# Optimization experiments

Hardware: AMD Instinct MI355X
Metric: run time of the kernel (lower is better)

The kernel has to match this reference:

```python
import jax, jax.numpy as jnp
import numpy as np

N_NODES = 2000
N_EDGES = 40000
DILATION = 2
DC = 32  # dilation_channels
C_IN = 32  # in_channels (= gcn out_channels)


def setup_inputs() -> dict:
    key = jax.random.key(0)
    ks = jax.random.split(key, 8)
    x = jax.random.normal(ks[0], (4, 34, N_NODES, C_IN), jnp.float32)
    edge_index = jax.random.randint(ks[1], (2, N_EDGES), 0, N_NODES, dtype=jnp.int64)
    edge_weight = jax.random.uniform(ks[2], (N_EDGES,), jnp.float32)
    gate1_w = jax.random.normal(ks[3], (DC, C_IN, 1, 2), jnp.float32) * 0.1
    gate1_b = jnp.zeros((DC,), jnp.float32)
    gate2_w = jax.random.normal(ks[4], (DC, C_IN, 1, 2), jnp.float32) * 0.1
    gate2_b = jnp.zeros((DC,), jnp.float32)
    gcn_w = jax.random.normal(ks[5], (DC, C_IN), jnp.float32) * 0.1
    gcn_b = jnp.zeros((C_IN,), jnp.float32)
    return {"x": x, "edge_index": edge_index, "edge_weight": edge_weight,
            "gate1_w": gate1_w, "gate1_b": gate1_b,
            "gate2_w": gate2_w, "gate2_b": gate2_b,
            "gcn_w": gcn_w, "gcn_b": gcn_b}


def _gate_conv(x_nchw, w, b):
    # Conv2d(kernel=(1,2), dilation=DILATION), VALID padding -> acts on time (W) axis
    y = jax.lax.conv_general_dilated(
        x_nchw, w, window_strides=(1, 1), padding='VALID',
        rhs_dilation=(1, DILATION),
        dimension_numbers=('NCHW', 'OIHW', 'NCHW'))
    return y + b[None, :, None, None]


def reference(x, edge_index, edge_weight, gate1_w, gate1_b, gate2_w, gate2_b, gcn_w, gcn_b):
    B, T, N, C = x.shape
    xt = jnp.transpose(x, (0, 3, 2, 1))  # (B, C, N, T)
    g1 = jnp.tanh(_gate_conv(xt, gate1_w, gate1_b))      # (B, DC, N, T')
    g2 = jax.nn.sigmoid(_gate_conv(xt, gate2_w, gate2_b))
    g = g1 * g2
    Tp = g.shape[-1]
    h = jnp.transpose(g, (0, 3, 2, 1)).reshape(B * Tp, N, DC)  # (Bt, N, DC)

    # GCN normalization with self loops (PyG gcn_norm, add_self_loops=True)
    row, col = edge_index[0], edge_index[1]
    loop = jnp.arange(N, dtype=edge_index.dtype)
    row_f = jnp.concatenate([row, loop])
    col_f = jnp.concatenate([col, loop])
    w_f = jnp.concatenate([edge_weight, jnp.ones((N,), edge_weight.dtype)])
    deg = jax.ops.segment_sum(w_f, col_f, num_segments=N)
    dis = jnp.where(deg > 0, jax.lax.rsqrt(deg), 0.0)
    norm = dis[row_f] * w_f * dis[col_f]  # (E+N,)

    hw = jnp.einsum('bnd,de->bne', h, gcn_w)          # (Bt, N, C_IN)
    msgs = hw[:, row_f, :] * norm[None, :, None]      # (Bt, E+N, C_IN)
    out = jnp.zeros_like(hw).at[:, col_f, :].add(msgs) + gcn_b  # scatter over targets

    return out.reshape(B, Tp, N, C_IN)  # (B, T', N, in_channels)
```

## Files before the change

### kernel.cpp

```cpp
#include <hip/hip_runtime.h>
#include <hip/hip_bf16.h>

typedef short short8 __attribute__((ext_vector_type(8)));
typedef float floatx4 __attribute__((ext_vector_type(4)));
typedef unsigned short ushort8_t __attribute__((ext_vector_type(8)));

#define NN 2000
#define NE 40000
#define NB 4
#define T_IN 34
#define TP 32
#define NBT (NB * TP)
#define NPOS (NB * TP * NN)
#define CAP 96


__device__ inline unsigned short f2bf(float x) {
    unsigned int u = __float_as_uint(x);
    u = u + 0x7fff + ((u >> 16) & 1);
    return (unsigned short)(u >> 16);
}
__device__ inline void splitPair(float x0, float x1, unsigned& hi, unsigned& lo) {
    unsigned u0 = __float_as_uint(x0), u1 = __float_as_uint(x1);
    hi = __builtin_amdgcn_perm(u1, u0, 0x07060302u);
    float r0 = x0 - __uint_as_float(u0 & 0xffff0000u);
    float r1 = x1 - __uint_as_float(u1 & 0xffff0000u);
    lo = __builtin_amdgcn_perm(__float_as_uint(r1), __float_as_uint(r0), 0x07060302u);
}
__device__ inline void splitA8(const float* v, short8& hi, short8& lo) {
    union { unsigned u[4]; short8 s; } H, L;
#pragma unroll
    for (int j = 0; j < 4; ++j) {
        unsigned h_, l_;
        splitPair(v[2 * j], v[2 * j + 1], h_, l_);
        H.u[j] = h_; L.u[j] = l_;
    }
    hi = H.s; lo = L.s;
}

__global__ __launch_bounds__(256) void conv_deg_kernel(
        const float* __restrict__ x,
        const float* __restrict__ w1, const float* __restrict__ b1,
        const float* __restrict__ w2, const float* __restrict__ b2,
        unsigned short* __restrict__ h2,
        const int* __restrict__ row, const int* __restrict__ col,
        const float* __restrict__ ew,
        float* __restrict__ deg, int* __restrict__ cursor,
        int2* __restrict__ pcsr) {
    if (blockIdx.x >= 1000) {
        int e = (blockIdx.x - 1000) * 256 + threadIdx.x;
        if (e < NE) {
            int c = col[e], r = row[e];
            float w = ew[e];
            atomicAdd(&deg[c], w);
            int slot = atomicAdd(&cursor[c], 1);
            if (slot < CAP) pcsr[c * CAP + slot] = make_int2(r, __float_as_int(w));
        }
        return;
    }

    int l = threadIdx.x & 63;
    int w = threadIdx.x >> 6;
    int colL = l & 15, q = l >> 4;

    short8 Whi[2][2][2], Wlo[2][2][2];
#pragma unroll
    for (int g = 0; g < 2; ++g) {
        const float* wp = g ? w2 : w1;
#pragma unroll
        for (int d = 0; d < 2; ++d)
#pragma unroll
        for (int tap = 0; tap < 2; ++tap) {
            float wv[8];
#pragma unroll
            for (int j = 0; j < 8; ++j)
                wv[j] = wp[(d * 16 + colL) * 64 + (q * 8 + j) * 2 + tap];
            splitA8(wv, Whi[g][d][tap], Wlo[g][d][tap]);
        }
    }
    float bias[2][2] = { { b1[colL], b1[colL + 16] }, { b2[colL], b2[colL + 16] } };

    for (int i = 0; i < 4; ++i) {
        int tile = blockIdx.x * 16 + w * 4 + i;
        int pos0 = tile * 16;
        int bt = pos0 / 2000;
        int n0 = pos0 - bt * 2000;
        int b_ = bt >> 5, t_ = bt & 31;
        const float* xa = x + (((b_ * T_IN + t_) * NN) + n0 + colL) * 32 + q * 8;
        const float* xb = xa + 2 * NN * 32;
        float va[8], vb[8];
        *(float4*)va       = *(const float4*)xa;
        *(float4*)(va + 4) = *(const float4*)(xa + 4);
        *(float4*)vb       = *(const float4*)xb;
        *(float4*)(vb + 4) = *(const float4*)(xb + 4);
        short8 Ahi0, Alo0, Ahi1, Alo1;
        splitA8(va, Ahi0, Alo0);
        splitA8(vb, Ahi1, Alo1);

        floatx4 acc[2][2];
#pragma unroll
        for (int g = 0; g < 2; ++g)
#pragma unroll
        for (int d = 0; d < 2; ++d) {
            float bv = bias[g][d];
            floatx4 a = { bv, bv, bv, bv };
            a = __builtin_amdgcn_mfma_f32_16x16x32_bf16(Ahi0, Whi[g][d][0], a, 0, 0, 0);
            a = __builtin_amdgcn_mfma_f32_16x16x32_bf16(Ahi1, Whi[g][d][1], a, 0, 0, 0);
            a = __builtin_amdgcn_mfma_f32_16x16x32_bf16(Alo0, Whi[g][d][0], a, 0, 0, 0);
            a = __builtin_amdgcn_mfma_f32_16x16x32_bf16(Alo1, Whi[g][d][1], a, 0, 0, 0);
            a = __builtin_amdgcn_mfma_f32_16x16x32_bf16(Ahi0, Wlo[g][d][0], a, 0, 0, 0);
            a = __builtin_amdgcn_mfma_f32_16x16x32_bf16(Ahi1, Wlo[g][d][1], a, 0, 0, 0);
            acc[g][d] = a;
        }

#pragma unroll
        for (int d = 0; d < 2; ++d)
#pragma unroll
        for (int r = 0; r < 4; ++r) {
            float g1 = acc[0][d][r];
            float g2 = acc[1][d][r];
            float e2 = __expf(2.0f * g1);
            float th = (e2 - 1.0f) / (e2 + 1.0f);
            float sg = 1.0f / (1.0f + __expf(-g2));
            float h = th * sg;
            int n = n0 + q * 4 + r;
            h2[(n * NBT + bt) * 32 + d * 16 + colL] = f2bf(h);
        }
    }
}

__device__ inline void acc8(float2* a2, const ushort8_t& v, float nr) {
    union { ushort8_t s; unsigned u[4]; } U; U.s = v;
#pragma unroll
    for (int j = 0; j < 4; ++j) {
        float2 vv;
        vv.x = __uint_as_float(U.u[j] << 16);
        vv.y = __uint_as_float(U.u[j] & 0xffff0000u);
        a2[j].x += vv.x * nr;
        a2[j].y += vv.y * nr;
    }
}

__global__ __launch_bounds__(256) void agg_gcn_kernel(
        const unsigned short* __restrict__ h2,
        const float* __restrict__ deg, const int* __restrict__ cursor,
        const int2* __restrict__ pcsr,
        const float* __restrict__ gw, const float* __restrict__ gb,
        float* __restrict__ out) {
    __shared__ float st[64 * 36];
    int l = threadIdx.x & 63;
    int wv = threadIdx.x >> 6;
    int b = blockIdx.x;
    int cp = b & 7;
    int n = (b >> 3) * 4 + wv;
    int colL = l & 15, q = l >> 4;

    short8 Bhi[2], Blo[2];
#pragma unroll
    for (int d = 0; d < 2; ++d) {
        float wv8[8];
#pragma unroll
        for (int j = 0; j < 8; ++j)
            wv8[j] = gw[(q * 8 + j) * 32 + d * 16 + colL];
        splitA8(wv8, Bhi[d], Blo[d]);
    }
    float gb0 = gb[colL], gb1 = gb[colL + 16];

    const unsigned short* base = h2 + cp * 512 + l * 8;
    float dn = rsqrtf(deg[n] + 1.0f);
    float w0 = dn * dn;
    float2 a2[4] = { {0,0}, {0,0}, {0,0}, {0,0} };
    {
        ushort8_t sv = *(const ushort8_t*)(base + (size_t)n * 4096);
        acc8(a2, sv, w0);
    }
    int cnt = cursor[n]; if (cnt > CAP) cnt = CAP;
    const int2* slots = pcsr + n * CAP;
    int i = 0;
    for (; i + 8 <= cnt; i += 8) {
        int2 e0 = slots[i],     e1 = slots[i + 1], e2 = slots[i + 2], e3 = slots[i + 3];
        int2 e4 = slots[i + 4], e5 = slots[i + 5], e6 = slots[i + 6], e7 = slots[i + 7];
        float n0 = rsqrtf(deg[e0.x] + 1.0f) * __int_as_float(e0.y) * dn;
        float n1 = rsqrtf(deg[e1.x] + 1.0f) * __int_as_float(e1.y) * dn;
        float n2 = rsqrtf(deg[e2.x] + 1.0f) * __int_as_float(e2.y) * dn;
        float n3 = rsqrtf(deg[e3.x] + 1.0f) * __int_as_float(e3.y) * dn;
        float n4 = rsqrtf(deg[e4.x] + 1.0f) * __int_as_float(e4.y) * dn;
        float n5 = rsqrtf(deg[e5.x] + 1.0f) * __int_as_float(e5.y) * dn;
        float n6 = rsqrtf(deg[e6.x] + 1.0f) * __int_as_float(e6.y) * dn;
        float n7 = rsqrtf(deg[e7.x] + 1.0f) * __int_as_float(e7.y) * dn;
        ushort8_t v0 = *(const ushort8_t*)(base + (size_t)e0.x * 4096);
        ushort8_t v1 = *(const ushort8_t*)(base + (size_t)e1.x * 4096);
        ushort8_t v2 = *(const ushort8_t*)(base + (size_t)e2.x * 4096);
        ushort8_t v3 = *(const ushort8_t*)(base + (size_t)e3.x * 4096);
        ushort8_t v4 = *(const ushort8_t*)(base + (size_t)e4.x * 4096);
        ushort8_t v5 = *(const ushort8_t*)(base + (size_t)e5.x * 4096);
        ushort8_t v6 = *(const ushort8_t*)(base + (size_t)e6.x * 4096);
        ushort8_t v7 = *(const ushort8_t*)(base + (size_t)e7.x * 4096);
        acc8(a2, v0, n0); acc8(a2, v1, n1); acc8(a2, v2, n2); acc8(a2, v3, n3);
        acc8(a2, v4, n4); acc8(a2, v5, n5); acc8(a2, v6, n6); acc8(a2, v7, n7);
    }
    for (; i + 4 <= cnt; i += 4) {
        int2 e0 = slots[i], e1 = slots[i + 1], e2 = slots[i + 2], e3 = slots[i + 3];
        float n0 = rsqrtf(deg[e0.x] + 1.0f) * __int_as_float(e0.y) * dn;
        float n1 = rsqrtf(deg[e1.x] + 1.0f) * __int_as_float(e1.y) * dn;
        float n2 = rsqrtf(deg[e2.x] + 1.0f) * __int_as_float(e2.y) * dn;
        float n3 = rsqrtf(deg[e3.x] + 1.0f) * __int_as_float(e3.y) * dn;
        ushort8_t v0 = *(const ushort8_t*)(base + (size_t)e0.x * 4096);
        ushort8_t v1 = *(const ushort8_t*)(base + (size_t)e1.x * 4096);
        ushort8_t v2 = *(const ushort8_t*)(base + (size_t)e2.x * 4096);
        ushort8_t v3 = *(const ushort8_t*)(base + (size_t)e3.x * 4096);
        acc8(a2, v0, n0); acc8(a2, v1, n1); acc8(a2, v2, n2); acc8(a2, v3, n3);
    }
    for (; i < cnt; ++i) {
        int2 e0 = slots[i];
        float n0 = rsqrtf(deg[e0.x] + 1.0f) * __int_as_float(e0.y) * dn;
        ushort8_t v0 = *(const ushort8_t*)(base + (size_t)e0.x * 4096);
        acc8(a2, v0, n0);
    }

    float* dst = &st[(wv * 16 + (l >> 2)) * 36 + (l & 3) * 8];
    *(float4*)dst       = make_float4(a2[0].x, a2[0].y, a2[1].x, a2[1].y);
    *(float4*)(dst + 4) = make_float4(a2[2].x, a2[2].y, a2[3].x, a2[3].y);
    __syncthreads();

    float av[8];
    const float* ap = &st[(wv * 16 + colL) * 36 + q * 8];
    *(float4*)av       = *(const float4*)ap;
    *(float4*)(av + 4) = *(const float4*)(ap + 4);
    short8 Ahi, Alo;
    splitA8(av, Ahi, Alo);
    floatx4 z = { 0.f, 0.f, 0.f, 0.f };
    floatx4 acc0 = z, acc1 = z;
    acc0 = __builtin_amdgcn_mfma_f32_16x16x32_bf16(Ahi, Bhi[0], acc0, 0, 0, 0);
    acc0 = __builtin_amdgcn_mfma_f32_16x16x32_bf16(Alo, Bhi[0], acc0, 0, 0, 0);
    acc0 = __builtin_amdgcn_mfma_f32_16x16x32_bf16(Ahi, Blo[0], acc0, 0, 0, 0);
    acc1 = __builtin_amdgcn_mfma_f32_16x16x32_bf16(Ahi, Bhi[1], acc1, 0, 0, 0);
    acc1 = __builtin_amdgcn_mfma_f32_16x16x32_bf16(Alo, Bhi[1], acc1, 0, 0, 0);
    acc1 = __builtin_amdgcn_mfma_f32_16x16x32_bf16(Ahi, Blo[1], acc1, 0, 0, 0);
#pragma unroll
    for (int r = 0; r < 4; ++r) {
        int btl = q * 4 + r;
        size_t o = ((size_t)(cp * 16 + btl) * NN + n) << 5;
        out[o + colL]      = acc0[r] + gb0;
        out[o + colL + 16] = acc1[r] + gb1;
    }
}

extern "C" void kernel_launch(void* const* d_in, const int* in_sizes, int n_in,
                              void* d_out, int out_size, void* d_ws, size_t ws_size,
                              hipStream_t stream) {
    const float* x   = (const float*)d_in[0];
    const int*   ei  = (const int*)d_in[1];
    const float* ew  = (const float*)d_in[2];
    const float* g1w = (const float*)d_in[3];
    const float* g1b = (const float*)d_in[4];
    const float* g2w = (const float*)d_in[5];
    const float* g2b = (const float*)d_in[6];
    const float* gcw = (const float*)d_in[7];
    const float* gcb = (const float*)d_in[8];
    float* out = (float*)d_out;

    float* wsf      = (float*)d_ws;
    float* deg      = wsf;
    int*   cursor   = (int*)(wsf + 2048);
    int2*  pcsr     = (int2*)(wsf + 4096);
    unsigned short* h2 = (unsigned short*)(wsf + 388096);

    const int* row = ei;
    const int* col = ei + NE;

    hipMemsetAsync(wsf, 0, 4096 * sizeof(float), stream);
    hipLaunchKernelGGL(conv_deg_kernel, dim3(1157), dim3(256), 0, stream,
                       x, g1w, g1b, g2w, g2b, h2, row, col, ew,
                       deg, cursor, pcsr);
    hipLaunchKernelGGL(agg_gcn_kernel, dim3(4000), dim3(256), 0, stream,
                       h2, deg, cursor, pcsr, gcw, gcb, out);
}
```

Baseline: 146.2 us.

## Reuse time-shifted input loads in gate conv and pack bf16 pairs

Each conv wave now walks 8 consecutive time steps for one node tile, keeping a 3-slot ring of loaded and bf16-split input rows. The dilated tap at t+2 is reused as the first tap two steps later, which removes roughly half of the global loads and split work. The edge-bucketing blocks move to the front of the grid. h2 stores channel pairs as packed 32-bit words, and the aggregation loop uses packed FMA (v_pk_fma_f32) with an adjusted shared-memory layout. The cost is fewer conv blocks with more serial work per wave, plus some register pressure from the ring.

```diff
diff --git a/kernel.cpp b/kernel.cpp
--- a/kernel.cpp
+++ b/kernel.cpp
@@ -3,7 +3,8 @@
 
 typedef short short8 __attribute__((ext_vector_type(8)));
 typedef float floatx4 __attribute__((ext_vector_type(4)));
-typedef unsigned short ushort8_t __attribute__((ext_vector_type(8)));
+typedef float float2v __attribute__((ext_vector_type(2)));
+typedef unsigned uint4v __attribute__((ext_vector_type(4)));
 
 #define NN 2000
 #define NE 40000
@@ -11,8 +12,8 @@
 #define T_IN 34
 #define TP 32
 #define NBT (NB * TP)
-#define NPOS (NB * TP * NN)
 #define CAP 96
+#define NEB 157
 
 
 __device__ inline unsigned short f2bf(float x) {
@@ -42,13 +43,13 @@
         const float* __restrict__ x,
         const float* __restrict__ w1, const float* __restrict__ b1,
         const float* __restrict__ w2, const float* __restrict__ b2,
-        unsigned short* __restrict__ h2,
+        unsigned* __restrict__ h2,
         const int* __restrict__ row, const int* __restrict__ col,
         const float* __restrict__ ew,
         float* __restrict__ deg, int* __restrict__ cursor,
         int2* __restrict__ pcsr) {
-    if (blockIdx.x >= 1000) {
-        int e = (blockIdx.x - 1000) * 256 + threadIdx.x;
+    if (blockIdx.x < NEB) {
+        int e = blockIdx.x * 256 + threadIdx.x;
         if (e < NE) {
             int c = col[e], r = row[e];
             float w = ew[e];
@@ -80,22 +81,32 @@
     }
     float bias[2][2] = { { b1[colL], b1[colL + 16] }, { b2[colL], b2[colL + 16] } };
 
-    for (int i = 0; i < 4; ++i) {
-        int tile = blockIdx.x * 16 + w * 4 + i;
-        int pos0 = tile * 16;
-        int bt = pos0 / 2000;
-        int n0 = pos0 - bt * 2000;
-        int b_ = bt >> 5, t_ = bt & 31;
-        const float* xa = x + (((b_ * T_IN + t_) * NN) + n0 + colL) * 32 + q * 8;
-        const float* xb = xa + 2 * NN * 32;
-        float va[8], vb[8];
-        *(float4*)va       = *(const float4*)xa;
-        *(float4*)(va + 4) = *(const float4*)(xa + 4);
-        *(float4*)vb       = *(const float4*)xb;
-        *(float4*)(vb + 4) = *(const float4*)(xb + 4);
-        short8 Ahi0, Alo0, Ahi1, Alo1;
-        splitA8(va, Ahi0, Alo0);
-        splitA8(vb, Ahi1, Alo1);
+    int cb = blockIdx.x - NEB;
+    int ntile = cb % 125;
+    int b_ = cb / 125;
+    int tb = w;
+    int n0 = ntile * 16;
+    int t0 = tb * 8;
+
+    const float* xw = x + (((size_t)b_ * T_IN * NN) + n0 + colL) * 32 + q * 8;
+    auto LD = [&](int t, float* vdst) {
+        const float* p = xw + (size_t)t * (NN * 32);
+        *(float4*)vdst       = *(const float4*)p;
+        *(float4*)(vdst + 4) = *(const float4*)(p + 4);
+    };
+
+    float v[3][8];
+    short8 shi[3], slo[3];
+    LD(t0, v[0]); LD(t0 + 1, v[1]); LD(t0 + 2, v[2]);
+    splitA8(v[0], shi[0], slo[0]);
+    splitA8(v[1], shi[1], slo[1]);
+
+#pragma unroll
+    for (int j = 0; j < 8; ++j) {
+        const int c0 = j % 3;
+        const int c2 = (j + 2) % 3;
+        splitA8(v[c2], shi[c2], slo[c2]);
+        if (j < 7) LD(t0 + j + 3, v[c0]);
 
         floatx4 acc[2][2];
 #pragma unroll
@@ -104,45 +115,45 @@
         for (int d = 0; d < 2; ++d) {
             float bv = bias[g][d];
             floatx4 a = { bv, bv, bv, bv };
-            a = __builtin_amdgcn_mfma_f32_16x16x32_bf16(Ahi0, Whi[g][d][0], a, 0, 0, 0);
-            a = __builtin_amdgcn_mfma_f32_16x16x32_bf16(Ahi1, Whi[g][d][1], a, 0, 0, 0);
-            a = __builtin_amdgcn_mfma_f32_16x16x32_bf16(Alo0, Whi[g][d][0], a, 0, 0, 0);
-            a = __builtin_amdgcn_mfma_f32_16x16x32_bf16(Alo1, Whi[g][d][1], a, 0, 0, 0);
-            a = __builtin_amdgcn_mfma_f32_16x16x32_bf16(Ahi0, Wlo[g][d][0], a, 0, 0, 0);
-            a = __builtin_amdgcn_mfma_f32_16x16x32_bf16(Ahi1, Wlo[g][d][1], a, 0, 0, 0);
+            a = __builtin_amdgcn_mfma_f32_16x16x32_bf16(shi[c0], Whi[g][d][0], a, 0, 0, 0);
+            a = __builtin_amdgcn_mfma_f32_16x16x32_bf16(shi[c2], Whi[g][d][1], a, 0, 0, 0);
+            a = __builtin_amdgcn_mfma_f32_16x16x32_bf16(slo[c0], Whi[g][d][0], a, 0, 0, 0);
+            a = __builtin_amdgcn_mfma_f32_16x16x32_bf16(slo[c2], Whi[g][d][1], a, 0, 0, 0);
+            a = __builtin_amdgcn_mfma_f32_16x16x32_bf16(shi[c0], Wlo[g][d][0], a, 0, 0, 0);
+            a = __builtin_amdgcn_mfma_f32_16x16x32_bf16(shi[c2], Wlo[g][d][1], a, 0, 0, 0);
             acc[g][d] = a;
         }
 
-#pragma unroll
-        for (int d = 0; d < 2; ++d)
+        int bt = b_ * TP + t0 + j;
 #pragma unroll
         for (int r = 0; r < 4; ++r) {
-            float g1 = acc[0][d][r];
-            float g2 = acc[1][d][r];
-            float e2 = __expf(2.0f * g1);
-            float th = (e2 - 1.0f) / (e2 + 1.0f);
-            float sg = 1.0f / (1.0f + __expf(-g2));
-            float h = th * sg;
+            float g10 = acc[0][0][r], g20 = acc[1][0][r];
+            float g11 = acc[0][1][r], g21 = acc[1][1][r];
+            float e20 = __expf(2.0f * g10);
+            float th0 = (e20 - 1.0f) / (e20 + 1.0f);
+            float sg0 = 1.0f / (1.0f + __expf(-g20));
+            float e21 = __expf(2.0f * g11);
+            float th1 = (e21 - 1.0f) / (e21 + 1.0f);
+            float sg1 = 1.0f / (1.0f + __expf(-g21));
+            unsigned pk = (unsigned)f2bf(th0 * sg0) | ((unsigned)f2bf(th1 * sg1) << 16);
             int n = n0 + q * 4 + r;
-            h2[(n * NBT + bt) * 32 + d * 16 + colL] = f2bf(h);
-        }
-    }
-}
-
-__device__ inline void acc8(float2* a2, const ushort8_t& v, float nr) {
-    union { ushort8_t s; unsigned u[4]; } U; U.s = v;
+            h2[(n * NBT + bt) * 16 + colL] = pk;
+        }
+    }
+}
+
+__device__ inline void acc8(float2v* a2, uint4v u, float2v nr2) {
 #pragma unroll
     for (int j = 0; j < 4; ++j) {
-        float2 vv;
-        vv.x = __uint_as_float(U.u[j] << 16);
-        vv.y = __uint_as_float(U.u[j] & 0xffff0000u);
-        a2[j].x += vv.x * nr;
-        a2[j].y += vv.y * nr;
+        float2v vv;
+        vv.x = __uint_as_float(u[j] << 16);
+        vv.y = __uint_as_float(u[j] & 0xffff0000u);
+        asm("v_pk_fma_f32 %0, %1, %2, %0" : "+v"(a2[j]) : "v"(vv), "v"(nr2));
     }
 }
 
 __global__ __launch_bounds__(256) void agg_gcn_kernel(
-        const unsigned short* __restrict__ h2,
+        const unsigned* __restrict__ h2,
         const float* __restrict__ deg, const int* __restrict__ cursor,
         const int2* __restrict__ pcsr,
         const float* __restrict__ gw, const float* __restrict__ gb,
@@ -166,13 +177,13 @@
     }
     float gb0 = gb[colL], gb1 = gb[colL + 16];
 
-    const unsigned short* base = h2 + cp * 512 + l * 8;
+    const unsigned* base = h2 + cp * 256 + l * 4;
     float dn = rsqrtf(deg[n] + 1.0f);
-    float w0 = dn * dn;
-    float2 a2[4] = { {0,0}, {0,0}, {0,0}, {0,0} };
+    float2v a2[4] = { {0,0}, {0,0}, {0,0}, {0,0} };
     {
-        ushort8_t sv = *(const ushort8_t*)(base + (size_t)n * 4096);
-        acc8(a2, sv, w0);
+        float w0 = dn * dn;
+        uint4v sv = *(const uint4v*)(base + (size_t)n * 2048);
+        acc8(a2, sv, (float2v){ w0, w0 });
     }
     int cnt = cursor[n]; if (cnt > CAP) cnt = CAP;
     const int2* slots = pcsr + n * CAP;
@@ -188,16 +199,18 @@
         float n5 = rsqrtf(deg[e5.x] + 1.0f) * __int_as_float(e5.y) * dn;
         float n6 = rsqrtf(deg[e6.x] + 1.0f) * __int_as_float(e6.y) * dn;
         float n7 = rsqrtf(deg[e7.x] + 1.0f) * __int_as_float(e7.y) * dn;
-        ushort8_t v0 = *(const ushort8_t*)(base + (size_t)e0.x * 4096);
-        ushort8_t v1 = *(const ushort8_t*)(base + (size_t)e1.x * 4096);
-        ushort8_t v2 = *(const ushort8_t*)(base + (size_t)e2.x * 4096);
-        ushort8_t v3 = *(const ushort8_t*)(base + (size_t)e3.x * 4096);
-        ushort8_t v4 = *(const ushort8_t*)(base + (size_t)e4.x * 4096);
-        ushort8_t v5 = *(const ushort8_t*)(base + (size_t)e5.x * 4096);
-        ushort8_t v6 = *(const ushort8_t*)(base + (size_t)e6.x * 4096);
-        ushort8_t v7 = *(const ushort8_t*)(base + (size_t)e7.x * 4096);
-        acc8(a2, v0, n0); acc8(a2, v1, n1); acc8(a2, v2, n2); acc8(a2, v3, n3);
-        acc8(a2, v4, n4); acc8(a2, v5, n5); acc8(a2, v6, n6); acc8(a2, v7, n7);
+        uint4v v0 = *(const uint4v*)(base + (size_t)e0.x * 2048);
+        uint4v v1 = *(const uint4v*)(base + (size_t)e1.x * 2048);
+        uint4v v2 = *(const uint4v*)(base + (size_t)e2.x * 2048);
+        uint4v v3 = *(const uint4v*)(base + (size_t)e3.x * 2048);
+        uint4v v4 = *(const uint4v*)(base + (size_t)e4.x * 2048);
+        uint4v v5 = *(const uint4v*)(base + (size_t)e5.x * 2048);
+        uint4v v6 = *(const uint4v*)(base + (size_t)e6.x * 2048);
+        uint4v v7 = *(const uint4v*)(base + (size_t)e7.x * 2048);
+        acc8(a2, v0, (float2v){n0, n0}); acc8(a2, v1, (float2v){n1, n1});
+        acc8(a2, v2, (float2v){n2, n2}); acc8(a2, v3, (float2v){n3, n3});
+        acc8(a2, v4, (float2v){n4, n4}); acc8(a2, v5, (float2v){n5, n5});
+        acc8(a2, v6, (float2v){n6, n6}); acc8(a2, v7, (float2v){n7, n7});
     }
     for (; i + 4 <= cnt; i += 4) {
         int2 e0 = slots[i], e1 = slots[i + 1], e2 = slots[i + 2], e3 = slots[i + 3];
@@ -205,22 +218,23 @@
         float n1 = rsqrtf(deg[e1.x] + 1.0f) * __int_as_float(e1.y) * dn;
         float n2 = rsqrtf(deg[e2.x] + 1.0f) * __int_as_float(e2.y) * dn;
         float n3 = rsqrtf(deg[e3.x] + 1.0f) * __int_as_float(e3.y) * dn;
-        ushort8_t v0 = *(const ushort8_t*)(base + (size_t)e0.x * 4096);
-        ushort8_t v1 = *(const ushort8_t*)(base + (size_t)e1.x * 4096);
-        ushort8_t v2 = *(const ushort8_t*)(base + (size_t)e2.x * 4096);
-        ushort8_t v3 = *(const ushort8_t*)(base + (size_t)e3.x * 4096);
-        acc8(a2, v0, n0); acc8(a2, v1, n1); acc8(a2, v2, n2); acc8(a2, v3, n3);
+        uint4v v0 = *(const uint4v*)(base + (size_t)e0.x * 2048);
+        uint4v v1 = *(const uint4v*)(base + (size_t)e1.x * 2048);
+        uint4v v2 = *(const uint4v*)(base + (size_t)e2.x * 2048);
+        uint4v v3 = *(const uint4v*)(base + (size_t)e3.x * 2048);
+        acc8(a2, v0, (float2v){n0, n0}); acc8(a2, v1, (float2v){n1, n1});
+        acc8(a2, v2, (float2v){n2, n2}); acc8(a2, v3, (float2v){n3, n3});
     }
     for (; i < cnt; ++i) {
         int2 e0 = slots[i];
         float n0 = rsqrtf(deg[e0.x] + 1.0f) * __int_as_float(e0.y) * dn;
-        ushort8_t v0 = *(const ushort8_t*)(base + (size_t)e0.x * 4096);
-        acc8(a2, v0, n0);
-    }
-
-    float* dst = &st[(wv * 16 + (l >> 2)) * 36 + (l & 3) * 8];
-    *(float4*)dst       = make_float4(a2[0].x, a2[0].y, a2[1].x, a2[1].y);
-    *(float4*)(dst + 4) = make_float4(a2[2].x, a2[2].y, a2[3].x, a2[3].y);
+        uint4v v0 = *(const uint4v*)(base + (size_t)e0.x * 2048);
+        acc8(a2, v0, (float2v){n0, n0});
+    }
+
+    float* dst = &st[(wv * 16 + (l >> 2)) * 36 + (l & 3) * 4];
+    *(float4*)dst        = make_float4(a2[0].x, a2[1].x, a2[2].x, a2[3].x);
+    *(float4*)(dst + 16) = make_float4(a2[0].y, a2[1].y, a2[2].y, a2[3].y);
     __syncthreads();
 
     float av[8];
@@ -264,13 +278,13 @@
     float* deg      = wsf;
     int*   cursor   = (int*)(wsf + 2048);
     int2*  pcsr     = (int2*)(wsf + 4096);
-    unsigned short* h2 = (unsigned short*)(wsf + 388096);
+    unsigned* h2    = (unsigned*)(wsf + 388096);
 
     const int* row = ei;
     const int* col = ei + NE;
 
     hipMemsetAsync(wsf, 0, 4096 * sizeof(float), stream);
-    hipLaunchKernelGGL(conv_deg_kernel, dim3(1157), dim3(256), 0, stream,
+    hipLaunchKernelGGL(conv_deg_kernel, dim3(NEB + 500), dim3(256), 0, stream,
                        x, g1w, g1b, g2w, g2b, h2, row, col, ew,
                        deg, cursor, pcsr);
     hipLaunchKernelGGL(agg_gcn_kernel, dim3(4000), dim3(256), 0, stream,
```

Measured after the change: 150.7 us. 3.1% more time.
